# Optimization experiments

Measured on AMD Instinct MI355X. Metric: run time of the kernel, lower is better.

## Reference

```python
import math
import jax, jax.numpy as jnp
import numpy as np

B, T, D_MODEL = 4, 2048, 1024
H, HD = 16, 64            # head_dim = d_model // n_heads
NF = 128                  # n_features
EPS = 1e-6
INV_SQRT_NF = 1.0 / math.sqrt(NF)


def make_orf(key, head_dim, n_features, dtype=jnp.float32):
    """Orthogonal Random Features: QR-orthogonalized gaussian blocks, scaled by sqrt(d)."""
    n_blocks = math.ceil(n_features / head_dim)
    keys = jax.random.split(key, n_blocks)
    blocks = []
    for k in keys:
        g = jax.random.normal(k, (head_dim, head_dim), dtype)
        qm, _ = jnp.linalg.qr(g)
        blocks.append(qm)
    W = jnp.concatenate(blocks, axis=1)[:, :n_features]
    return W * jnp.asarray(math.sqrt(head_dim), dtype)


def setup_inputs() -> dict:
    key = jax.random.key(0)
    k0, k1, k2, k3, k4, k5 = jax.random.split(key, 6)
    s = 1.0 / math.sqrt(D_MODEL)  # torch Linear default init scale
    x = jax.random.normal(k0, (B, T, D_MODEL), jnp.float32)
    Wq = jax.random.uniform(k1, (D_MODEL, H * HD), jnp.float32, -s, s)
    Wk = jax.random.uniform(k2, (D_MODEL, H * HD), jnp.float32, -s, s)
    Wv = jax.random.uniform(k3, (D_MODEL, H * HD), jnp.float32, -s, s)
    Wo = jax.random.uniform(k4, (H * HD, D_MODEL), jnp.float32, -s, s)
    W_feat = make_orf(k5, HD, NF)  # (HD, NF), fresh random buffer (not learned)
    return {"x": x, "Wq": Wq, "Wk": Wk, "Wv": Wv, "Wo": Wo, "W_feat": W_feat}


def _favor_plus(x, W):
    """phi(x) = exp(x.W - ||x||^2/2) / sqrt(NF); x:(B,H,T,HD) -> (B,H,T,NF)."""
    sq = 0.5 * jnp.sum(x * x, axis=-1, keepdims=True)
    return jnp.exp(x @ W - sq) * INV_SQRT_NF


def _causal_linear_attention(qp, kp, v):
    """Causal linear attention scan. qp,kp:(B,H,T,NF), v:(B,H,T,HD) -> (B,H,T,HD)."""
    Bb, Hh = qp.shape[0], qp.shape[1]

    def step(carry, qkv):
        S, z = carry  # S:(B,H,NF,HD), z:(B,H,NF)
        q_t, k_t, v_t = qkv
        S = S + jnp.einsum('bhd,bhe->bhde', k_t, v_t)
        z = z + k_t
        num = jnp.einsum('bhd,bhde->bhe', q_t, S)
        den = jnp.einsum('bhd,bhd->bh', q_t, z) + EPS
        return (S, z), num / den[..., None]

    S0 = jnp.zeros((Bb, Hh, NF, HD), qp.dtype)
    z0 = jnp.zeros((Bb, Hh, NF), qp.dtype)
    xs = (jnp.moveaxis(qp, 2, 0), jnp.moveaxis(kp, 2, 0), jnp.moveaxis(v, 2, 0))
    _, ys = jax.lax.scan(step, (S0, z0), xs)  # ys: (T,B,H,HD)
    return jnp.moveaxis(ys, 0, 2)  # (B,H,T,HD)


def reference(x, Wq, Wk, Wv, Wo, W_feat):
    Bb, Tt, _ = x.shape

    def heads(W):
        return (x @ W).reshape(Bb, Tt, H, HD).transpose(0, 2, 1, 3)  # (B,H,T,HD)

    q, k, v = heads(Wq), heads(Wk), heads(Wv)
    qp = _favor_plus(q, W_feat)
    kp = _favor_plus(k, W_feat)
    y = _causal_linear_attention(qp, kp, v)           # (B,H,T,HD)
    y = y.transpose(0, 2, 1, 3).reshape(Bb, Tt, H * HD)
    return y @ Wo
```

## Files before the change

### kernel.cpp

```cpp
#include <hip/hip_runtime.h>
#include <hip/hip_bf16.h>

typedef unsigned int u32;
typedef unsigned short u16;
typedef __bf16 bf16x8 __attribute__((ext_vector_type(8)));
typedef float f32x4 __attribute__((ext_vector_type(4)));

__device__ __forceinline__ float b2f(u16 s){ union{u32 x; float f;} c; c.x = ((u32)s) << 16; return c.f; }
__device__ __forceinline__ float b2f_lo(u32 u){ union{u32 x; float f;} c; c.x = u << 16; return c.f; }
__device__ __forceinline__ float b2f_hi(u32 u){ union{u32 x; float f;} c; c.x = u & 0xFFFF0000u; return c.f; }
__device__ __forceinline__ u16 f2b(float f){
    union{float f; u32 u;} c; c.f = f;
    u32 r = c.u + 0x7FFFu + ((c.u >> 16) & 1u);
    return (u16)(r >> 16);
}
__device__ __forceinline__ u32 pk(float lo, float hi){
    return (u32)f2b(lo) | ((u32)f2b(hi) << 16);
}
__device__ __forceinline__ void gl_lds16(const u16* g, u16* l){
    __builtin_amdgcn_global_load_lds(
        (const __attribute__((address_space(1))) void*)g,
        (__attribute__((address_space(3))) void*)l, 16, 0, 0);
}
#define BARRIER() do { __builtin_amdgcn_s_barrier(); asm volatile("" ::: "memory"); } while(0)
#define SCB __builtin_amdgcn_sched_barrier(0)
#define PHASE_GATE() do { asm volatile("" ::: "memory"); __builtin_amdgcn_s_barrier(); \
    asm volatile("s_waitcnt lgkmcnt(0)" ::: "memory"); SCB; } while(0)
#define LD8(p) (*reinterpret_cast<const bf16x8*>(p))


__global__ __launch_bounds__(256) void tobf16(const float* __restrict__ in, u16* __restrict__ out)
{
    size_t i = ((size_t)blockIdx.x * 256 + threadIdx.x) * 8;
    float4 a = *reinterpret_cast<const float4*>(in + i);
    float4 b = *reinterpret_cast<const float4*>(in + i + 4);
    uint4 v; v.x = pk(a.x, a.y); v.y = pk(a.z, a.w); v.z = pk(b.x, b.y); v.w = pk(b.z, b.w);
    *reinterpret_cast<uint4*>(out + i) = v;
}

__global__ __launch_bounds__(256) void transpose_all(const float* __restrict__ Wq, const float* __restrict__ Wk,
                                                     const float* __restrict__ Wv, const float* __restrict__ Wo,
                                                     u16* __restrict__ WTqkv, u16* __restrict__ WTo)
{
    const float* in; u16* out;
    switch (blockIdx.z){
        case 0:  in = Wq; out = WTqkv;           break;
        case 1:  in = Wk; out = WTqkv + 1048576; break;
        case 2:  in = Wv; out = WTqkv + 2097152; break;
        default: in = Wo; out = WTo;             break;
    }
    __shared__ u16 tile[64][72];
    int kb = blockIdx.x * 64, nb = blockIdx.y * 64, tid = threadIdx.x;
#pragma unroll
    for (int i = 0; i < 2; i++){
        int idx = tid + 256*i; int r = idx >> 3; int c8 = (idx & 7) * 8;
        const float* p = &in[(size_t)(kb + r)*1024 + nb + c8];
        float4 lo = *reinterpret_cast<const float4*>(p);
        float4 hi = *reinterpret_cast<const float4*>(p + 4);
        uint4 v;
        v.x = pk(lo.x, lo.y); v.y = pk(lo.z, lo.w);
        v.z = pk(hi.x, hi.y); v.w = pk(hi.z, hi.w);
        *reinterpret_cast<uint4*>(&tile[r][c8]) = v;
    }
    __syncthreads();
#pragma unroll
    for (int i = 0; i < 2; i++){
        int idx = tid + 256*i; int c = idx >> 3; int r8 = (idx & 7) * 8;
        u32 w[4];
#pragma unroll
        for (int j = 0; j < 4; j++)
            w[j] = (u32)tile[r8 + 2*j][c] | ((u32)tile[r8 + 2*j + 1][c] << 16);
        uint4 v; v.x = w[0]; v.y = w[1]; v.z = w[2]; v.w = w[3];
        *reinterpret_cast<uint4*>(&out[(size_t)(nb + c)*1024 + kb + r8]) = v;
    }
}

template<int MODE>
__global__ __launch_bounds__(512, 2) void gemm_2p(const u16* __restrict__ A, const u16* __restrict__ BT,
                                                  float* __restrict__ outf, u16* __restrict__ outh)
{
    __shared__ u16 lds[2][24576];
    const int tid = threadIdx.x;
    const int l = tid & 63, w = tid >> 6;
    const int wr = w >> 2, wc = w & 3;
    const int fr = l & 15, q = l >> 4;
    const int m0 = blockIdx.x * 128, n0 = blockIdx.y * 256;

    const int srow = tid >> 3;
    const int scol = ((tid & 7) ^ (srow & 7)) << 3;
    const u16* Ag = A  + (size_t)(m0 + srow) * 1024 + scol;
    const u16* Bg = BT + (size_t)(n0 + srow) * 1024 + scol;
    const int sd = tid * 8;

    const int colk0 = (q*8)      ^ ((fr & 7) << 3);
    const int colk1 = (32 + q*8) ^ ((fr & 7) << 3);
    const int aoff = (wr*64 + fr) * 64;
    const int boff = 8192 + (wc*64 + fr) * 64;

    f32x4 acc[4][4] = {};
    bf16x8 af[4][2], bf[2][2];

    auto stgA = [&](int buf, int kt){
#pragma unroll
        for (int i = 0; i < 2; ++i)
            gl_lds16(Ag + (size_t)(i*64)*1024 + kt*64, &lds[buf][i*4096 + sd]);
    };
    auto stgB = [&](int buf, int kt){
#pragma unroll
        for (int j = 0; j < 4; ++j)
            gl_lds16(Bg + (size_t)(j*64)*1024 + kt*64, &lds[buf][8192 + j*4096 + sd]);
    };

    stgA(0, 0); stgB(0, 0); stgA(1, 1);
    asm volatile("s_waitcnt vmcnt(2)" ::: "memory");
    SCB;
    BARRIER();

#pragma unroll 1
    for (int uu = 0; uu < 8; ++uu){
        const bool s = (uu < 7);

#pragma unroll
        for (int par = 0; par < 2; ++par){
            u16* Lb = &lds[par][0];
            const int ktB = 2*uu + 1 + par;
            const int ktA = 2*uu + 2 + par;
            const bool sB = (par == 0) ? true : s;
            const bool sA = s;

#pragma unroll
            for (int mt = 0; mt < 4; ++mt){
                af[mt][0] = LD8(Lb + aoff + mt*1024 + colk0);
                af[mt][1] = LD8(Lb + aoff + mt*1024 + colk1);
            }
#pragma unroll
            for (int nt = 0; nt < 2; ++nt){
                bf[nt][0] = LD8(Lb + boff + nt*1024 + colk0);
                bf[nt][1] = LD8(Lb + boff + nt*1024 + colk1);
            }
            if (sB) stgB(par ^ 1, ktB);
            PHASE_GATE();
            __builtin_amdgcn_s_setprio(1);
#pragma unroll
            for (int mt = 0; mt < 4; ++mt)
#pragma unroll
                for (int nt = 0; nt < 2; ++nt){
                    acc[mt][nt] = __builtin_amdgcn_mfma_f32_16x16x32_bf16(af[mt][0], bf[nt][0], acc[mt][nt], 0, 0, 0);
                    acc[mt][nt] = __builtin_amdgcn_mfma_f32_16x16x32_bf16(af[mt][1], bf[nt][1], acc[mt][nt], 0, 0, 0);
                }
            __builtin_amdgcn_s_setprio(0);
            SCB;
            BARRIER();

#pragma unroll
            for (int nt = 0; nt < 2; ++nt){
                bf[nt][0] = LD8(Lb + boff + (2+nt)*1024 + colk0);
                bf[nt][1] = LD8(Lb + boff + (2+nt)*1024 + colk1);
            }
            if (sA) stgA(par, ktA);
            PHASE_GATE();
            __builtin_amdgcn_s_setprio(1);
#pragma unroll
            for (int mt = 0; mt < 4; ++mt)
#pragma unroll
                for (int nt = 0; nt < 2; ++nt){
                    acc[mt][2+nt] = __builtin_amdgcn_mfma_f32_16x16x32_bf16(af[mt][0], bf[nt][0], acc[mt][2+nt], 0, 0, 0);
                    acc[mt][2+nt] = __builtin_amdgcn_mfma_f32_16x16x32_bf16(af[mt][1], bf[nt][1], acc[mt][2+nt], 0, 0, 0);
                }
            __builtin_amdgcn_s_setprio(0);
            SCB;
            if (sA) asm volatile("s_waitcnt vmcnt(2)" ::: "memory");
            else    asm volatile("s_waitcnt vmcnt(0)" ::: "memory");
            SCB;
            BARRIER();
        }
    }

#pragma unroll
    for (int mt = 0; mt < 4; ++mt){
        int row0 = m0 + wr*64 + mt*16 + q*4;
#pragma unroll
        for (int nt = 0; nt < 4; ++nt){
            int col = n0 + wc*64 + nt*16 + fr;
#pragma unroll
            for (int r = 0; r < 4; ++r){
                float val = acc[mt][nt][r];
                int row = row0 + r;
                if (MODE == 2){
                    outf[(size_t)row*1024 + col] = val;
                } else {
                    int which = col >> 10, colw = col & 1023;
                    int h = colw >> 6, d = colw & 63;
                    int bb = row >> 11, tt = row & 2047;
                    outh[(size_t)which*8388608 + (((size_t)(bb*16 + h))*2048 + tt)*64 + d] = f2b(val);
                }
            }
        }
    }
}

__global__ __launch_bounds__(256) void featmap_mfma(const u16* __restrict__ xh, const float* __restrict__ Wf,
                                                    u16* __restrict__ xp)
{
    __shared__ u16 Xl[128][72];
    __shared__ u16 Wft[128][72];
    __shared__ float sqp[128][8];
    __shared__ float sql[128];
    int tid = threadIdx.x;
    int lane = tid & 63, w = tid >> 6;
    int m = lane & 15, q = lane >> 4;
    const u16* xb = xh + (size_t)blockIdx.x * 128 * 64;
#pragma unroll
    for (int it = 0; it < 4; it++){
        int idx = tid + 256*it;
        int row = idx >> 3, c8 = (idx & 7) * 8;
        uint4 v = *reinterpret_cast<const uint4*>(xb + (size_t)row*64 + c8);
        *reinterpret_cast<uint4*>(&Xl[row][c8]) = v;
        u32 ww[4] = {v.x, v.y, v.z, v.w};
        float s = 0.f;
#pragma unroll
        for (int j = 0; j < 4; j++){
            float a = b2f_lo(ww[j]), bb = b2f_hi(ww[j]);
            s += a*a + bb*bb;
        }
        sqp[row][idx & 7] = s;
    }
#pragma unroll
    for (int it = 0; it < 8; it++){
        int idx = tid + 256*it;
        int d = idx >> 5, f4 = (idx & 31) * 4;
        float4 v = *reinterpret_cast<const float4*>(Wf + d*128 + f4);
        Wft[f4+0][d] = f2b(v.x); Wft[f4+1][d] = f2b(v.y);
        Wft[f4+2][d] = f2b(v.z); Wft[f4+3][d] = f2b(v.w);
    }
    __syncthreads();
    if (tid < 128){
        float s = 0.f;
#pragma unroll
        for (int j = 0; j < 8; j++) s += sqp[tid][j];
        sql[tid] = s;
    }
    f32x4 acc[2][8] = {};
#pragma unroll
    for (int ks = 0; ks < 2; ks++){
        bf16x8 af[2], bf[8];
#pragma unroll
        for (int mt = 0; mt < 2; mt++)
            af[mt] = *reinterpret_cast<const bf16x8*>(&Xl[32*w + mt*16 + m][ks*32 + q*8]);
#pragma unroll
        for (int nt = 0; nt < 8; nt++)
            bf[nt] = *reinterpret_cast<const bf16x8*>(&Wft[nt*16 + m][ks*32 + q*8]);
#pragma unroll
        for (int mt = 0; mt < 2; mt++)
#pragma unroll
            for (int nt = 0; nt < 8; nt++)
                acc[mt][nt] = __builtin_amdgcn_mfma_f32_16x16x32_bf16(af[mt], bf[nt], acc[mt][nt], 0, 0, 0);
    }
    __syncthreads();
    const float c = 0.08838834764831845f;
    u16* xpb = xp + (size_t)blockIdx.x * 128 * 128;
#pragma unroll
    for (int mt = 0; mt < 2; mt++){
#pragma unroll
        for (int r = 0; r < 4; r++){
            int t = 32*w + mt*16 + q*4 + r;
            float hs = 0.5f * sql[t];
#pragma unroll
            for (int nt = 0; nt < 8; nt++){
                int f = nt*16 + m;
                xpb[(size_t)t*128 + f] = f2b(__expf(fminf(acc[mt][nt][r] - hs, 60.f)) * c);
            }
        }
    }
}

struct FM1 { u16 Xl[128][72]; u16 Wft[128][72]; };
union  FMU { FM1 p1; u16 Kpt[128][136]; };
__global__ __launch_bounds__(256) void featmap_sum(const u16* __restrict__ kh, const float* __restrict__ Wf,
                                                   const u16* __restrict__ vh, u16* __restrict__ kp,
                                                   u16* __restrict__ Sa, float* __restrict__ zs)
{
    __shared__ FMU sm;
    __shared__ u16 Vt[64][136];
    __shared__ float sqp[128][8];
    __shared__ float sql[128];
    int blk = blockIdx.x, tid = threadIdx.x;
    int lane = tid & 63, w = tid >> 6;
    int m = lane & 15, q = lane >> 4;
    const u16* xb = kh + (size_t)blk * 128 * 64;
    const u16* vb = vh + (size_t)blk * 128 * 64;
#pragma unroll
    for (int it = 0; it < 4; it++){
        int idx = tid + 256*it;
        int row = idx >> 3, c8 = (idx & 7) * 8;
        uint4 v = *reinterpret_cast<const uint4*>(xb + (size_t)row*64 + c8);
        *reinterpret_cast<uint4*>(&sm.p1.Xl[row][c8]) = v;
        u32 ww[4] = {v.x, v.y, v.z, v.w};
        float s = 0.f;
#pragma unroll
        for (int j = 0; j < 4; j++){
            float a = b2f_lo(ww[j]), bb = b2f_hi(ww[j]);
            s += a*a + bb*bb;
        }
        sqp[row][idx & 7] = s;
    }
#pragma unroll
    for (int it = 0; it < 8; it++){
        int idx = tid + 256*it;
        int d = idx >> 5, f4 = (idx & 31) * 4;
        float4 v = *reinterpret_cast<const float4*>(Wf + d*128 + f4);
        sm.p1.Wft[f4+0][d] = f2b(v.x); sm.p1.Wft[f4+1][d] = f2b(v.y);
        sm.p1.Wft[f4+2][d] = f2b(v.z); sm.p1.Wft[f4+3][d] = f2b(v.w);
    }
#pragma unroll
    for (int it = 0; it < 4; it++){
        int idx = tid + 256*it;
        int t = idx >> 3, d8 = (idx & 7)*8;
        uint4 v = *reinterpret_cast<const uint4*>(vb + (size_t)t*64 + d8);
        u32 ww[4] = {v.x, v.y, v.z, v.w};
#pragma unroll
        for (int j = 0; j < 4; j++){
            Vt[d8 + 2*j][t]     = (u16)(ww[j] & 0xFFFFu);
            Vt[d8 + 2*j + 1][t] = (u16)(ww[j] >> 16);
        }
    }
    __syncthreads();
    if (tid < 128){
        float s = 0.f;
#pragma unroll
        for (int j = 0; j < 8; j++) s += sqp[tid][j];
        sql[tid] = s;
    }
    f32x4 acc[2][8] = {};
#pragma unroll
    for (int ks = 0; ks < 2; ks++){
        bf16x8 af[2], bf[8];
#pragma unroll
        for (int mt = 0; mt < 2; mt++)
            af[mt] = *reinterpret_cast<const bf16x8*>(&sm.p1.Xl[32*w + mt*16 + m][ks*32 + q*8]);
#pragma unroll
        for (int nt = 0; nt < 8; nt++)
            bf[nt] = *reinterpret_cast<const bf16x8*>(&sm.p1.Wft[nt*16 + m][ks*32 + q*8]);
#pragma unroll
        for (int mt = 0; mt < 2; mt++)
#pragma unroll
            for (int nt = 0; nt < 8; nt++)
                acc[mt][nt] = __builtin_amdgcn_mfma_f32_16x16x32_bf16(af[mt], bf[nt], acc[mt][nt], 0, 0, 0);
    }
    __syncthreads();
    const float c = 0.08838834764831845f;
    u16* xpb = kp + (size_t)blk * 128 * 128;
#pragma unroll
    for (int mt = 0; mt < 2; mt++){
#pragma unroll
        for (int r = 0; r < 4; r++){
            int t = 32*w + mt*16 + q*4 + r;
            float hs = 0.5f * sql[t];
#pragma unroll
            for (int nt = 0; nt < 8; nt++){
                int f = nt*16 + m;
                u16 pv = f2b(__expf(fminf(acc[mt][nt][r] - hs, 60.f)) * c);
                xpb[(size_t)t*128 + f] = pv;
                sm.Kpt[f][t] = pv;
            }
        }
    }
    __syncthreads();
    f32x4 acc2[8] = {};
#pragma unroll
    for (int ks = 0; ks < 4; ks++){
        bf16x8 af = *reinterpret_cast<const bf16x8*>(&Vt[16*w + m][ks*32 + q*8]);
        bf16x8 bf[8];
#pragma unroll
        for (int nt = 0; nt < 8; nt++)
            bf[nt] = *reinterpret_cast<const bf16x8*>(&sm.Kpt[nt*16 + m][ks*32 + q*8]);
#pragma unroll
        for (int nt = 0; nt < 8; nt++)
            acc2[nt] = __builtin_amdgcn_mfma_f32_16x16x32_bf16(af, bf[nt], acc2[nt], 0, 0, 0);
    }
    u16* Sb = Sa + (size_t)blk*8192;
#pragma unroll
    for (int nt = 0; nt < 8; nt++){
#pragma unroll
        for (int r = 0; r < 4; r++){
            int d = 16*w + q*4 + r;
            int f = nt*16 + m;
            Sb[(size_t)d*128 + f] = f2b(acc2[nt][r]);
        }
    }
    if (tid < 128){
        float z = 0.f;
#pragma unroll
        for (int t = 0; t < 128; t++) z += b2f(sm.Kpt[tid][t]);
        zs[(size_t)blk*128 + tid] = z;
    }
}

__global__ __launch_bounds__(256) void prefix_chunks(const u16* __restrict__ Sa, u16* __restrict__ Sb,
                                                     float* __restrict__ zs)
{
    int bh = blockIdx.x, seg = blockIdx.y, tid = threadIdx.x;
    const u16* src = Sa + (size_t)bh*16*8192;
    u16*       dst = Sb + (size_t)bh*16*8192;
#pragma unroll
    for (int it = 0; it < 4; it++){
        int e = seg*1024 + it*256 + tid;
        float run = 0.f;
#pragma unroll
        for (int c = 0; c < 16; c++){
            float v = b2f(src[(size_t)c*8192 + e]);
            dst[(size_t)c*8192 + e] = f2b(run);
            run += v;
        }
    }
    if (seg == 0 && tid < 128){
        float run = 0.f; float* zp = zs + (size_t)bh*16*128 + tid;
#pragma unroll
        for (int c = 0; c < 16; c++){ float v = zp[c*128]; zp[c*128] = run; run += v; }
    }
}

__global__ __launch_bounds__(256) void chunk_out(const u16* __restrict__ qp, const u16* __restrict__ kp,
                                                 const u16* __restrict__ vh, const u16* __restrict__ St,
                                                 const float* __restrict__ zs, u16* __restrict__ y2d)
{
    __shared__ u16 P[128][136];
    __shared__ u16 Vt[64][136];
    __shared__ u16 zl[128];
    int blk = blockIdx.x, tid = threadIdx.x;
    int lane = tid & 63, w = tid >> 6;
    int m = lane & 15, q = lane >> 4;
    int bh = blk >> 4, c = blk & 15;
    int b = bh >> 4, h = bh & 15, t0 = c*128;
    const u16* qpb = qp + ((size_t)bh*2048 + t0)*128;
    const u16* kpb = kp + ((size_t)bh*2048 + t0)*128;
    const u16* vb  = vh + ((size_t)bh*2048 + t0)*64;
    const u16* Stb = St + (size_t)blk*8192;

    if (tid < 128) zl[tid] = f2b(zs[(size_t)blk*128 + tid]);
#pragma unroll
    for (int it = 0; it < 4; it++){
        int idx = tid + 256*it;
        int t = idx >> 3, d8 = (idx & 7)*8;
        uint4 v = *reinterpret_cast<const uint4*>(&vb[(size_t)t*64 + d8]);
        u32 ww[4] = {v.x, v.y, v.z, v.w};
#pragma unroll
        for (int j = 0; j < 4; j++){
            Vt[d8 + 2*j][t]     = (u16)(ww[j] & 0xFFFFu);
            Vt[d8 + 2*j + 1][t] = (u16)(ww[j] >> 16);
        }
    }
    {
        int row = tid >> 1, half = tid & 1;
        int i = row >> 4;
        for (int s2 = 16*(i + 1) + half*2; s2 < 128; s2 += 4)
            *reinterpret_cast<u32*>(&P[row][s2]) = 0;
    }
    {
        static const unsigned char TIa[36] = {0,1,1,2,2,2,3,3,3,3,4,4,4,4,4,
                                              5,5,5,5,5,5,6,6,6,6,6,6,6,7,7,7,7,7,7,7,7};
        static const unsigned char TJa[36] = {0,0,1,0,1,2,0,1,2,3,0,1,2,3,4,
                                              0,1,2,3,4,5,0,1,2,3,4,5,6,0,1,2,3,4,5,6,7};
        for (int idx = w; idx < 36; idx += 4){
            int i = TIa[idx], j = TJa[idx];
            f32x4 a = {};
            const u16* arow = qpb + (size_t)(i*16 + m)*128 + q*8;
            const u16* brow = kpb + (size_t)(j*16 + m)*128 + q*8;
#pragma unroll
            for (int ks = 0; ks < 4; ks++){
                bf16x8 af = *reinterpret_cast<const bf16x8*>(arow + ks*32);
                bf16x8 bf = *reinterpret_cast<const bf16x8*>(brow + ks*32);
                a = __builtin_amdgcn_mfma_f32_16x16x32_bf16(af, bf, a, 0, 0, 0);
            }
            int scol = j*16 + m;
#pragma unroll
            for (int r = 0; r < 4; r++){
                int trow = i*16 + q*4 + r;
                P[trow][scol] = (scol <= trow) ? f2b(a[r]) : (u16)0;
            }
        }
    }
    __syncthreads();
    f32x4 acc[2][4] = {};
    f32x4 accd[2] = {};
    bf16x8 ones;
#pragma unroll
    for (int i = 0; i < 8; i++) ones[i] = (__bf16)1.0f;
    for (int ks = 0; ks <= w; ks++){
        bf16x8 af[2], bf4[4];
#pragma unroll
        for (int mt = 0; mt < 2; mt++)
            af[mt] = *reinterpret_cast<const bf16x8*>(&P[32*w + mt*16 + m][ks*32 + q*8]);
#pragma unroll
        for (int nt = 0; nt < 4; nt++)
            bf4[nt] = *reinterpret_cast<const bf16x8*>(&Vt[nt*16 + m][ks*32 + q*8]);
#pragma unroll
        for (int mt = 0; mt < 2; mt++){
#pragma unroll
            for (int nt = 0; nt < 4; nt++)
                acc[mt][nt] = __builtin_amdgcn_mfma_f32_16x16x32_bf16(af[mt], bf4[nt], acc[mt][nt], 0, 0, 0);
            accd[mt] = __builtin_amdgcn_mfma_f32_16x16x32_bf16(af[mt], ones, accd[mt], 0, 0, 0);
        }
    }
#pragma unroll
    for (int ks = 0; ks < 4; ks++){
        bf16x8 af[2], bf4[4];
        bf16x8 zf = *reinterpret_cast<const bf16x8*>(&zl[ks*32 + q*8]);
#pragma unroll
        for (int mt = 0; mt < 2; mt++)
            af[mt] = *reinterpret_cast<const bf16x8*>(qpb + (size_t)(32*w + mt*16 + m)*128 + ks*32 + q*8);
#pragma unroll
        for (int nt = 0; nt < 4; nt++)
            bf4[nt] = *reinterpret_cast<const bf16x8*>(Stb + (size_t)(nt*16 + m)*128 + ks*32 + q*8);
#pragma unroll
        for (int mt = 0; mt < 2; mt++){
#pragma unroll
            for (int nt = 0; nt < 4; nt++)
                acc[mt][nt] = __builtin_amdgcn_mfma_f32_16x16x32_bf16(af[mt], bf4[nt], acc[mt][nt], 0, 0, 0);
            accd[mt] = __builtin_amdgcn_mfma_f32_16x16x32_bf16(af[mt], zf, accd[mt], 0, 0, 0);
        }
    }
#pragma unroll
    for (int mt = 0; mt < 2; mt++){
#pragma unroll
        for (int nt = 0; nt < 4; nt++){
#pragma unroll
            for (int r = 0; r < 4; r++){
                int t = 32*w + mt*16 + q*4 + r;
                int d = nt*16 + m;
                float den = accd[mt][r] + 1e-6f;
                y2d[((size_t)b*2048 + t0 + t)*1024 + h*64 + d] = f2b(acc[mt][nt][r] / den);
            }
        }
    }
}

extern "C" void kernel_launch(void* const* d_in, const int* in_sizes, int n_in,
                              void* d_out, int out_size, void* d_ws, size_t ws_size,
                              hipStream_t stream)
{
    (void)in_sizes; (void)n_in; (void)out_size; (void)ws_size;
    const float* x  = (const float*)d_in[0];
    const float* Wq = (const float*)d_in[1];
    const float* Wk = (const float*)d_in[2];
    const float* Wv = (const float*)d_in[3];
    const float* Wo = (const float*)d_in[4];
    const float* Wf = (const float*)d_in[5];
    float* out = (float*)d_out;
    char* ws = (char*)d_ws;

    u16*   xh    = (u16*)  (ws + 0);
    u16*   Sa    = (u16*)  (ws + 0);
    u16*   qh    = (u16*)  (ws + 16777216);
    u16*   Sbp   = (u16*)  (ws + 16777216);
    u16*   kh    = (u16*)  (ws + 33554432);
    u16*   y2d   = (u16*)  (ws + 33554432);
    u16*   vh    = (u16*)  (ws + 50331648);
    u16*   qp    = (u16*)  (ws + 67108864);
    u16*   kp    = (u16*)  (ws + 100663296);
    u16*   WTqkv = (u16*)  (ws + 134217728);
    u16*   WTo   = (u16*)  (ws + 140509184);
    float* zs    = (float*)(ws + 142606336);

    tobf16<<<4096, 256, 0, stream>>>(x, xh);
    transpose_all<<<dim3(16, 16, 4), 256, 0, stream>>>(Wq, Wk, Wv, Wo, WTqkv, WTo);

    gemm_2p<3><<<dim3(64, 12), 512, 0, stream>>>(xh, WTqkv, nullptr, qh);

    featmap_mfma<<<1024, 256, 0, stream>>>(qh, Wf, qp);
    featmap_sum<<<1024, 256, 0, stream>>>(kh, Wf, vh, kp, Sa, zs);

    prefix_chunks<<<dim3(64, 8), 256, 0, stream>>>(Sa, Sbp, zs);
    chunk_out<<<1024, 256, 0, stream>>>(qp, kp, vh, Sbp, zs, y2d);

    gemm_2p<2><<<dim3(64, 4), 512, 0, stream>>>(y2d, WTo, out, nullptr);
}
```

Measured before the change: 292.9 us.

## Double chunk_out threads to 512 and XOR-swizzle LDS tiles instead of padding

chunk_out now runs 8 waves per block, each owning 16 rows of the 128-token chunk instead of 32, which halves per-wave accumulators and spreads the intra-chunk QK^T tiles across more waves. The padded LDS arrays P and Vt are replaced by unpadded ones indexed with an XOR swizzle on column groups, to avoid bank conflicts while using less shared memory. The cost is more threads per block and more per-row redundant global loads of St and zl. The diff relies on an LD8 helper that must be defined in the unseen part of the file.

```diff
diff --git a/kernel.cpp b/kernel.cpp
--- a/kernel.cpp
+++ b/kernel.cpp
@@ -420,12 +420,12 @@
     }
 }
 
-__global__ __launch_bounds__(256) void chunk_out(const u16* __restrict__ qp, const u16* __restrict__ kp,
+__global__ __launch_bounds__(512) void chunk_out(const u16* __restrict__ qp, const u16* __restrict__ kp,
                                                  const u16* __restrict__ vh, const u16* __restrict__ St,
                                                  const float* __restrict__ zs, u16* __restrict__ y2d)
 {
-    __shared__ u16 P[128][136];
-    __shared__ u16 Vt[64][136];
+    __shared__ u16 P[128][128];
+    __shared__ u16 Vt[64][128];
     __shared__ u16 zl[128];
     int blk = blockIdx.x, tid = threadIdx.x;
     int lane = tid & 63, w = tid >> 6;
@@ -436,101 +436,89 @@
     const u16* kpb = kp + ((size_t)bh*2048 + t0)*128;
     const u16* vb  = vh + ((size_t)bh*2048 + t0)*64;
     const u16* Stb = St + (size_t)blk*8192;
+    const int xm = (m & 7) << 3;
 
     if (tid < 128) zl[tid] = f2b(zs[(size_t)blk*128 + tid]);
 #pragma unroll
-    for (int it = 0; it < 4; it++){
-        int idx = tid + 256*it;
+    for (int it = 0; it < 2; it++){
+        int idx = tid + 512*it;
         int t = idx >> 3, d8 = (idx & 7)*8;
         uint4 v = *reinterpret_cast<const uint4*>(&vb[(size_t)t*64 + d8]);
         u32 ww[4] = {v.x, v.y, v.z, v.w};
 #pragma unroll
         for (int j = 0; j < 4; j++){
-            Vt[d8 + 2*j][t]     = (u16)(ww[j] & 0xFFFFu);
-            Vt[d8 + 2*j + 1][t] = (u16)(ww[j] >> 16);
+            Vt[d8 + 2*j]    [t ^ ((2*j)     << 3)] = (u16)(ww[j] & 0xFFFFu);
+            Vt[d8 + 2*j + 1][t ^ ((2*j + 1) << 3)] = (u16)(ww[j] >> 16);
         }
     }
     {
-        int row = tid >> 1, half = tid & 1;
-        int i = row >> 4;
-        for (int s2 = 16*(i + 1) + half*2; s2 < 128; s2 += 4)
-            *reinterpret_cast<u32*>(&P[row][s2]) = 0;
+        int row = tid >> 2, c4 = tid & 3;
+        int i = row >> 4, xr = (row & 7) << 3;
+        for (int s2 = 16*(i + 1) + c4*2; s2 < 128; s2 += 8)
+            *reinterpret_cast<u32*>(&P[row][s2 ^ xr]) = 0;
     }
     {
         static const unsigned char TIa[36] = {0,1,1,2,2,2,3,3,3,3,4,4,4,4,4,
                                               5,5,5,5,5,5,6,6,6,6,6,6,6,7,7,7,7,7,7,7,7};
         static const unsigned char TJa[36] = {0,0,1,0,1,2,0,1,2,3,0,1,2,3,4,
                                               0,1,2,3,4,5,0,1,2,3,4,5,6,0,1,2,3,4,5,6,7};
-        for (int idx = w; idx < 36; idx += 4){
+        for (int idx = w; idx < 36; idx += 8){
             int i = TIa[idx], j = TJa[idx];
             f32x4 a = {};
             const u16* arow = qpb + (size_t)(i*16 + m)*128 + q*8;
             const u16* brow = kpb + (size_t)(j*16 + m)*128 + q*8;
 #pragma unroll
             for (int ks = 0; ks < 4; ks++){
-                bf16x8 af = *reinterpret_cast<const bf16x8*>(arow + ks*32);
-                bf16x8 bf = *reinterpret_cast<const bf16x8*>(brow + ks*32);
+                bf16x8 af = LD8(arow + ks*32);
+                bf16x8 bf = LD8(brow + ks*32);
                 a = __builtin_amdgcn_mfma_f32_16x16x32_bf16(af, bf, a, 0, 0, 0);
             }
             int scol = j*16 + m;
 #pragma unroll
             for (int r = 0; r < 4; r++){
                 int trow = i*16 + q*4 + r;
-                P[trow][scol] = (scol <= trow) ? f2b(a[r]) : (u16)0;
-            }
-        }
-    }
-    __syncthreads();
-    f32x4 acc[2][4] = {};
-    f32x4 accd[2] = {};
+                P[trow][scol ^ ((trow & 7) << 3)] = (scol <= trow) ? f2b(a[r]) : (u16)0;
+            }
+        }
+    }
+    __syncthreads();
+    f32x4 acc4[4] = {};
+    f32x4 accd = {};
     bf16x8 ones;
 #pragma unroll
     for (int i = 0; i < 8; i++) ones[i] = (__bf16)1.0f;
-    for (int ks = 0; ks <= w; ks++){
-        bf16x8 af[2], bf4[4];
-#pragma unroll
-        for (int mt = 0; mt < 2; mt++)
-            af[mt] = *reinterpret_cast<const bf16x8*>(&P[32*w + mt*16 + m][ks*32 + q*8]);
+    for (int ks = 0; ks <= (w >> 1); ks++){
+        bf16x8 af = LD8(&P[16*w + m][(ks*32 + q*8) ^ xm]);
+        bf16x8 bf4[4];
 #pragma unroll
         for (int nt = 0; nt < 4; nt++)
-            bf4[nt] = *reinterpret_cast<const bf16x8*>(&Vt[nt*16 + m][ks*32 + q*8]);
-#pragma unroll
-        for (int mt = 0; mt < 2; mt++){
-#pragma unroll
-            for (int nt = 0; nt < 4; nt++)
-                acc[mt][nt] = __builtin_amdgcn_mfma_f32_16x16x32_bf16(af[mt], bf4[nt], acc[mt][nt], 0, 0, 0);
-            accd[mt] = __builtin_amdgcn_mfma_f32_16x16x32_bf16(af[mt], ones, accd[mt], 0, 0, 0);
-        }
+            bf4[nt] = LD8(&Vt[nt*16 + m][(ks*32 + q*8) ^ xm]);
+#pragma unroll
+        for (int nt = 0; nt < 4; nt++)
+            acc4[nt] = __builtin_amdgcn_mfma_f32_16x16x32_bf16(af, bf4[nt], acc4[nt], 0, 0, 0);
+        accd = __builtin_amdgcn_mfma_f32_16x16x32_bf16(af, ones, accd, 0, 0, 0);
     }
 #pragma unroll
     for (int ks = 0; ks < 4; ks++){
-        bf16x8 af[2], bf4[4];
-        bf16x8 zf = *reinterpret_cast<const bf16x8*>(&zl[ks*32 + q*8]);
-#pragma unroll
-        for (int mt = 0; mt < 2; mt++)
-            af[mt] = *reinterpret_cast<const bf16x8*>(qpb + (size_t)(32*w + mt*16 + m)*128 + ks*32 + q*8);
+        bf16x8 af = LD8(qpb + (size_t)(16*w + m)*128 + ks*32 + q*8);
+        bf16x8 zf = LD8(&zl[ks*32 + q*8]);
+        bf16x8 bf4[4];
 #pragma unroll
         for (int nt = 0; nt < 4; nt++)
-            bf4[nt] = *reinterpret_cast<const bf16x8*>(Stb + (size_t)(nt*16 + m)*128 + ks*32 + q*8);
-#pragma unroll
-        for (int mt = 0; mt < 2; mt++){
-#pragma unroll
-            for (int nt = 0; nt < 4; nt++)
-                acc[mt][nt] = __builtin_amdgcn_mfma_f32_16x16x32_bf16(af[mt], bf4[nt], acc[mt][nt], 0, 0, 0);
-            accd[mt] = __builtin_amdgcn_mfma_f32_16x16x32_bf16(af[mt], zf, accd[mt], 0, 0, 0);
-        }
-    }
-#pragma unroll
-    for (int mt = 0; mt < 2; mt++){
-#pragma unroll
-        for (int nt = 0; nt < 4; nt++){
-#pragma unroll
-            for (int r = 0; r < 4; r++){
-                int t = 32*w + mt*16 + q*4 + r;
-                int d = nt*16 + m;
-                float den = accd[mt][r] + 1e-6f;
-                y2d[((size_t)b*2048 + t0 + t)*1024 + h*64 + d] = f2b(acc[mt][nt][r] / den);
-            }
+            bf4[nt] = LD8(Stb + (size_t)(nt*16 + m)*128 + ks*32 + q*8);
+#pragma unroll
+        for (int nt = 0; nt < 4; nt++)
+            acc4[nt] = __builtin_amdgcn_mfma_f32_16x16x32_bf16(af, bf4[nt], acc4[nt], 0, 0, 0);
+        accd = __builtin_amdgcn_mfma_f32_16x16x32_bf16(af, zf, accd, 0, 0, 0);
+    }
+#pragma unroll
+    for (int nt = 0; nt < 4; nt++){
+#pragma unroll
+        for (int r = 0; r < 4; r++){
+            int t = 16*w + q*4 + r;
+            int d = nt*16 + m;
+            float den = accd[r] + 1e-6f;
+            y2d[((size_t)b*2048 + t0 + t)*1024 + h*64 + d] = f2b(acc4[nt][r] / den);
         }
     }
 }
@@ -571,7 +559,7 @@
     featmap_sum<<<1024, 256, 0, stream>>>(kh, Wf, vh, kp, Sa, zs);
 
     prefix_chunks<<<dim3(64, 8), 256, 0, stream>>>(Sa, Sbp, zs);
-    chunk_out<<<1024, 256, 0, stream>>>(qp, kp, vh, Sbp, zs, y2d);
+    chunk_out<<<1024, 512, 0, stream>>>(qp, kp, vh, Sbp, zs, y2d);
 
     gemm_2p<2><<<dim3(64, 4), 512, 0, stream>>>(y2d, WTo, out, nullptr);
 }
```

Result: faster. 282.6 us (-3.5%).
